# Kernel tuning notes

Hardware: AMD Instinct MI355X
Metric: run time of the kernel (lower is better)

## Reference

```python
import jax, jax.numpy as jnp
import numpy as np

N_QUBITS = 12
LAYERS = 2
BATCH = 1024


def _apply_1q(state, gate, q):
    # state: [B] + [2]*n (wire 0 = leading qubit axis); gate: [2,2] or [B,2,2]
    axis = 1 + q
    st = jnp.moveaxis(state, axis, -1)
    if gate.ndim == 2:
        st = jnp.einsum('ij,...j->...i', gate, st)
    else:  # batched gate (angle depends on the input sample)
        st = jnp.einsum('bij,b...j->b...i', gate, st)
    return jnp.moveaxis(st, -1, axis)


def _apply_cnot(state, c, t):
    # flip target axis on the control=1 slice
    ca, ta = 1 + c, 1 + t
    a0 = jnp.take(state, 0, axis=ca)
    a1 = jnp.take(state, 1, axis=ca)
    ta2 = ta - 1 if ta > ca else ta
    a1 = jnp.flip(a1, axis=ta2)
    return jnp.stack([a0, a1], axis=ca)


def _rx(a):
    # a: [B] -> gate [B,2,2]
    h = 0.5 * a
    c = jnp.cos(h).astype(jnp.complex64)
    s = (-1j) * jnp.sin(h).astype(jnp.complex64)
    return jnp.stack([jnp.stack([c, s], -1), jnp.stack([s, c], -1)], -2)


def _ry(a):
    h = 0.5 * a
    c = jnp.cos(h).astype(jnp.complex64)
    s = jnp.sin(h).astype(jnp.complex64)
    return jnp.stack([jnp.stack([c, -s], -1), jnp.stack([s, c], -1)], -2)


def _rz(a):
    h = 0.5 * a
    e0 = jnp.exp(-1j * h.astype(jnp.complex64))
    e1 = jnp.exp(1j * h.astype(jnp.complex64))
    z = jnp.zeros_like(e0)
    return jnp.stack([jnp.stack([e0, z], -1), jnp.stack([z, e1], -1)], -2)


def setup_inputs() -> dict:
    key = jax.random.key(0)
    k1, k2 = jax.random.split(key)
    x = jax.random.normal(k1, (BATCH, N_QUBITS), dtype=jnp.float32)
    theta = jax.random.normal(k2, (LAYERS, N_QUBITS, 2), dtype=jnp.float32)
    lam = jnp.ones((LAYERS, N_QUBITS), dtype=jnp.float32)
    return {"x": x, "theta": theta, "lam": lam}


def reference(x, theta, lam):
    B = x.shape[0]
    n = N_QUBITS
    # |0...0> state, batched: [B] + [2]*n
    state = jnp.zeros((B,) + (2,) * n, dtype=jnp.complex64)
    state = state.at[(slice(None),) + (0,) * n].set(1.0)
    for l in range(LAYERS):
        for q in range(n):
            state = _apply_1q(state, _rx(lam[l, q] * x[:, q]), q)
        for q in range(n):
            state = _apply_cnot(state, q, (q + 1) % n)
        for q in range(n):
            state = _apply_1q(state, _ry(theta[l, q, 0]), q)
            state = _apply_1q(state, _rz(theta[l, q, 1]), q)
    probs = state.real ** 2 + state.imag ** 2  # [B] + [2]*n
    zs = []
    for q in range(n):
        axes = tuple(i for i in range(1, n + 1) if i != 1 + q)
        p = jnp.sum(probs, axis=axes)  # [B, 2]
        zs.append(p[:, 0] - p[:, 1])   # <Z_q>
    return jnp.stack(zs, axis=1)  # [B, n_qubits]
```

## Files before the change

### kernel.cpp

```cpp
#include <hip/hip_runtime.h>
#include <math.h>

#define NQ 12
#define TPB 512


__device__ __forceinline__ int sg(int j) {
    return (j & ~15) | ((j ^ (j >> 4) ^ (j >> 8)) & 15);
}

__device__ __forceinline__ float2 pk_mul(float2 a, float2 b) {
    float2 d;
    asm("v_pk_mul_f32 %0, %1, %2" : "=v"(d) : "v"(a), "v"(b));
    return d;
}
__device__ __forceinline__ float2 pk_fma(float2 a, float2 b, float2 c) {
    float2 d;
    asm("v_pk_fma_f32 %0, %1, %2, %3" : "=v"(d) : "v"(a), "v"(b), "v"(c));
    return d;
}

#define FOR_PAIRS3(RB, STMT) do {                                     \
    const int msk_ = 1 << (RB);                                       \
    _Pragma("unroll")                                                 \
    for (int h_ = 0; h_ < 4; ++h_) {                                  \
        const int i0 = ((h_ & ~(msk_ - 1)) << 1) | (h_ & (msk_ - 1)); \
        const int i1 = i0 | msk_;                                     \
        STMT;                                                         \
    } } while (0)

#define J_A(r) (((r) << 9) | t)
#define J_B(r) (((t >> 6) << 9) | ((r) << 6) | (t & 63))
#define J_C(r) (((t >> 3) << 6) | ((r) << 3) | (t & 7))
#define J_D(r) ((t << 3) | (r))

#define LOCAL_X(JS, JD) do {                                          \
    _Pragma("unroll")                                                 \
    for (int r_ = 0; r_ < 8; ++r_) S[sg(JS(r_))] = v[r_];             \
    _Pragma("unroll")                                                 \
    for (int r_ = 0; r_ < 8; ++r_) v[r_] = S[sg(JD(r_))];             \
  } while (0)

#define M_GATE(q, RB) do {                                                  \
        float4 A4 = mA[q]; float2 P2 = mB[q];                               \
        float2 c2  = make_float2(A4.x, A4.x);                               \
        float2 s2  = make_float2(A4.y, A4.y);                               \
        float2 ms2 = make_float2(-A4.y, -A4.y);                             \
        FOR_PAIRS3(RB, {                                                    \
            float2 a1 = v[i1];                                              \
            float2 b1 = make_float2(A4.z*a1.x - A4.w*a1.y,                  \
                                    A4.z*a1.y + A4.w*a1.x);                 \
            float2 n0 = pk_fma(b1, ms2, pk_mul(v[i0], c2));                 \
            float2 n1 = pk_fma(v[i0], s2, pk_mul(b1, c2));                  \
            v[i0] = n0;                                                     \
            v[i1] = make_float2(P2.x*n1.x - P2.y*n1.y,                      \
                                P2.x*n1.y + P2.y*n1.x);                     \
        });                                                                 \
    } while (0)

#define RY_GATE(q, RB) do {                                                 \
        float2 cs = coY[q];                                                 \
        float2 c2  = make_float2(cs.x, cs.x);                               \
        float2 s2  = make_float2(cs.y, cs.y);                               \
        float2 ms2 = make_float2(-cs.y, -cs.y);                             \
        FOR_PAIRS3(RB, {                                                    \
            float2 n0 = pk_fma(v[i1], ms2, pk_mul(v[i0], c2));              \
            float2 n1 = pk_fma(v[i0], s2, pk_mul(v[i1], c2));               \
            v[i0] = n0; v[i1] = n1;                                         \
        });                                                                 \
    } while (0)

#define M_PHASE(QB)  do { _Pragma("unroll")                                 \
    for (int d_ = 0; d_ < 3; ++d_) M_GATE((QB) + d_, 2 - d_); } while (0)
#define RY_PHASE(QB) do { _Pragma("unroll")                                 \
    for (int d_ = 0; d_ < 3; ++d_) RY_GATE((QB) + d_, 2 - d_); } while (0)

__global__ __launch_bounds__(TPB) void vqc_kernel(
    const float* __restrict__ x,
    const float* __restrict__ th,
    const float* __restrict__ lm,
    float* __restrict__ out)
{
    __shared__ float2 S[4096];
    __shared__ float4 mA[12];
    __shared__ float2 mB[12];
    __shared__ float2 coI[12];
    __shared__ float2 coY[12];
    __shared__ float red[8 * 12];

    const int b = blockIdx.x;
    const int t = threadIdx.x;
    const int l = t & 63;
    const int w = t >> 6;

    if (t < 12) {
        float h = 0.5f * lm[t] * x[b * NQ + t];
        float c, s; __sincosf(h, &s, &c);
        coI[t] = make_float2(c, s);
    } else if (t < 24) {
        int q = t - 12;
        float h = 0.5f * th[24 + 2 * q];
        float c, s; __sincosf(h, &s, &c);
        coY[q] = make_float2(c, s);
    } else if (t < 36) {
        int q = t - 24;
        float ha = 0.5f * lm[12 + q] * x[b * NQ + q];
        float hy = 0.5f * th[2 * q];
        float hz = 0.5f * th[2 * q + 1];
        float ca, sa, cy, sy, cz, sz;
        __sincosf(ha, &sa, &ca);
        __sincosf(hy, &sy, &cy);
        __sincosf(hz, &sz, &cz);
        float ax = ca*cy*cz + sa*sy*sz;
        float ay = -(ca*cy*sz + sa*sy*cz);
        float bx = ca*sy*cz - sa*cy*sz;
        float by = ca*sy*sz - sa*cy*cz;
        float na = ax*ax + ay*ay, nb = bx*bx + by*by;
        float ra = rsqrtf(fmaxf(na, 1e-30f));
        float rb = rsqrtf(fmaxf(nb, 1e-30f));
        float ux = ax*ra, uy = ay*ra;
        float wx = bx*rb, wy = by*rb;
        mA[q] = make_float4(na*ra, nb*rb,
                            ux*wx - uy*wy, -(ux*wy + uy*wx));
        mB[q] = make_float2(ux*wx + uy*wy, ux*wy - uy*wx);
    }
    __syncthreads();

    float2 v[8];

    {
        const int g = (t ^ (t >> 1)) & 0x7F;
        float Pt = 1.0f;
#pragma unroll
        for (int m = 0; m < 7; ++m) {
            float2 cs = coI[8 - m];
            Pt *= ((g >> m) & 1) ? cs.y : cs.x;
        }
        const int ct = __popc(g);
        const int t0 = t & 1, t8 = (t >> 8) & 1;
        const int e1 = ((t >> 7) ^ (t >> 8)) & 1;
        float2 q11 = coI[11], q10 = coI[10], q9 = coI[9],
               q1 = coI[1], q0 = coI[0];
        const float u9  = t0 ? q9.y : q9.x;
        const float u9n = t0 ? q9.x : q9.y;
        const float u1  = e1 ? q1.y : q1.x;
        const float u1n = e1 ? q1.x : q1.y;
        const float u0  = t8 ? q0.y : q0.x;
        const float u0n = t8 ? q0.x : q0.y;
#pragma unroll
        for (int r = 0; r < 8; ++r) {
            const int r0 = r & 1, r1 = (r >> 1) & 1, r2 = (r >> 2) & 1;
            const int b11 = r0 ^ r1, b10 = r1 ^ r2;
            float m = Pt * (b11 ? q11.y : q11.x) * (b10 ? q10.y : q10.x)
                         * (r2 ? u9n : u9) * (r0 ? u1n : u1)
                         * (r0 ? u0n : u0);
            int k = (ct + b11 + b10 + (r2 ^ t0) + (r0 ^ e1) + (r0 ^ t8)) & 3;
            v[r].x = (k == 0) ? m : ((k == 2) ? -m : 0.0f);
            v[r].y = (k == 3) ? m : ((k == 1) ? -m : 0.0f);
        }
    }

    M_PHASE(9);
    LOCAL_X(J_D, J_C);
    M_PHASE(6);
    LOCAL_X(J_C, J_B);
    M_PHASE(3);
#pragma unroll
    for (int r = 0; r < 8; ++r) S[sg(J_B(r))] = v[r];
    __syncthreads();
#pragma unroll
    for (int r = 0; r < 8; ++r) v[r] = S[sg(J_A(r))];
    M_PHASE(0);

    __syncthreads();
#pragma unroll
    for (int r = 0; r < 8; ++r) {
        int j = J_A(r);
        int y = j ^ (j >> 1); y ^= y >> 2; y ^= y >> 4; y ^= y >> 8;
        int p = (y & 0x7FF) | (((__popc(j) ^ (j >> 11)) & 1) << 11);
        S[sg(p)] = v[r];
    }
    __syncthreads();
#pragma unroll
    for (int r = 0; r < 8; ++r) v[r] = S[sg(J_A(r))];

    RY_PHASE(0);
    __syncthreads();
#pragma unroll
    for (int r = 0; r < 8; ++r) S[sg(J_A(r))] = v[r];
    __syncthreads();
#pragma unroll
    for (int r = 0; r < 8; ++r) v[r] = S[sg(J_B(r))];
    RY_PHASE(3);
    LOCAL_X(J_B, J_C);
    RY_PHASE(6);
    LOCAL_X(J_C, J_D);
    RY_PHASE(9);

    float ptot = 0.f, z9 = 0.f, z10 = 0.f, z11 = 0.f;
#pragma unroll
    for (int r = 0; r < 8; ++r) {
        float p = fmaf(v[r].x, v[r].x, v[r].y * v[r].y);
        ptot += p;
        z9  += (r & 4) ? -p : p;
        z10 += (r & 2) ? -p : p;
        z11 += (r & 1) ? -p : p;
    }
    float vals[4] = {ptot, z9, z10, z11};
#pragma unroll
    for (int k = 0; k < 6; ++k) {
        const float sgn = ((l >> k) & 1) ? -1.f : 1.f;
#pragma unroll
        for (int m = 0; m < 4; ++m) {
            float tmp = __shfl_xor(vals[m], 1 << k, 64);
            vals[m] = fmaf(sgn, vals[m], tmp);
        }
    }
    if (l == 0) {
        red[w * 12 + 0]  = vals[0];
        red[w * 12 + 9]  = vals[1];
        red[w * 12 + 10] = vals[2];
        red[w * 12 + 11] = vals[3];
    } else if (__popc(l) == 1) {
        int q = 9 - __ffs(l);
        red[w * 12 + q] = vals[0];
    }
    __syncthreads();
    if (t < NQ) {
        float acc = 0.f;
#pragma unroll
        for (int ww = 0; ww < 8; ++ww) {
            float vv = red[ww * 12 + (t < 3 ? 0 : t)];
            if (t < 3) acc += ((ww >> (2 - t)) & 1) ? -vv : vv;
            else       acc += vv;
        }
        out[b * NQ + t] = acc;
    }
}

extern "C" void kernel_launch(void* const* d_in, const int* in_sizes, int n_in,
                              void* d_out, int out_size, void* d_ws, size_t ws_size,
                              hipStream_t stream) {
    const int B = in_sizes[0] / NQ;
    vqc_kernel<<<B, TPB, 0, stream>>>((const float*)d_in[0],
                                      (const float*)d_in[1],
                                      (const float*)d_in[2],
                                      (float*)d_out);
}
```

Before: 79.76 us.

## Halve block size to 256 threads with 16 amplitudes per thread

Each block now runs 256 threads, and each thread holds 16 complex amplitudes instead of 8. Each thread therefore applies four gates locally per phase, so the phases drop from four to three and one shared-memory exchange round disappears in each half. Gate coefficients are broadcast through readfirstlane so they live in scalar registers. The cost is more VGPR pressure per thread and fewer threads per block, which may lower occupancy or latency hiding.

Result: no change. 78.28 us (-1.9%).

```diff
diff --git a/kernel.cpp b/kernel.cpp
--- a/kernel.cpp
+++ b/kernel.cpp
@@ -2,11 +2,15 @@
 #include <math.h>
 
 #define NQ 12
-#define TPB 512
+#define TPB 256
 
 
 __device__ __forceinline__ int sg(int j) {
     return (j & ~15) | ((j ^ (j >> 4) ^ (j >> 8)) & 15);
+}
+
+__device__ __forceinline__ float rfl(float x) {
+    return __int_as_float(__builtin_amdgcn_readfirstlane(__float_as_int(x)));
 }
 
 __device__ __forceinline__ float2 pk_mul(float2 a, float2 b) {
@@ -20,50 +24,53 @@
     return d;
 }
 
-#define FOR_PAIRS3(RB, STMT) do {                                     \
+#define FOR_PAIRS4(RB, STMT) do {                                     \
     const int msk_ = 1 << (RB);                                       \
     _Pragma("unroll")                                                 \
-    for (int h_ = 0; h_ < 4; ++h_) {                                  \
+    for (int h_ = 0; h_ < 8; ++h_) {                                  \
         const int i0 = ((h_ & ~(msk_ - 1)) << 1) | (h_ & (msk_ - 1)); \
         const int i1 = i0 | msk_;                                     \
         STMT;                                                         \
     } } while (0)
 
-#define J_A(r) (((r) << 9) | t)
-#define J_B(r) (((t >> 6) << 9) | ((r) << 6) | (t & 63))
-#define J_C(r) (((t >> 3) << 6) | ((r) << 3) | (t & 7))
-#define J_D(r) ((t << 3) | (r))
+#define J_A(r) (((r) << 8) | t)
+#define J_B(r) (((t >> 4) << 8) | ((r) << 4) | (t & 15))
+#define J_C(r) ((t << 4) | (r))
 
 #define LOCAL_X(JS, JD) do {                                          \
     _Pragma("unroll")                                                 \
-    for (int r_ = 0; r_ < 8; ++r_) S[sg(JS(r_))] = v[r_];             \
+    for (int r_ = 0; r_ < 16; ++r_) S[sg(JS(r_))] = v[r_];            \
     _Pragma("unroll")                                                 \
-    for (int r_ = 0; r_ < 8; ++r_) v[r_] = S[sg(JD(r_))];             \
+    for (int r_ = 0; r_ < 16; ++r_) v[r_] = S[sg(JD(r_))];            \
   } while (0)
 
 #define M_GATE(q, RB) do {                                                  \
-        float4 A4 = mA[q]; float2 P2 = mB[q];                               \
-        float2 c2  = make_float2(A4.x, A4.x);                               \
-        float2 s2  = make_float2(A4.y, A4.y);                               \
-        float2 ms2 = make_float2(-A4.y, -A4.y);                             \
-        FOR_PAIRS3(RB, {                                                    \
+        float4 A4v = mA[q]; float2 P2v = mB[q];                             \
+        float az = rfl(A4v.z), aw = rfl(A4v.w);                             \
+        float px = rfl(P2v.x), py = rfl(P2v.y);                             \
+        float cth = rfl(A4v.x), sth = rfl(A4v.y);                           \
+        float2 c2  = make_float2(cth, cth);                                 \
+        float2 s2  = make_float2(sth, sth);                                 \
+        float2 ms2 = make_float2(-sth, -sth);                               \
+        FOR_PAIRS4(RB, {                                                    \
             float2 a1 = v[i1];                                              \
-            float2 b1 = make_float2(A4.z*a1.x - A4.w*a1.y,                  \
-                                    A4.z*a1.y + A4.w*a1.x);                 \
+            float2 b1 = make_float2(az*a1.x - aw*a1.y,                      \
+                                    az*a1.y + aw*a1.x);                     \
             float2 n0 = pk_fma(b1, ms2, pk_mul(v[i0], c2));                 \
             float2 n1 = pk_fma(v[i0], s2, pk_mul(b1, c2));                  \
             v[i0] = n0;                                                     \
-            v[i1] = make_float2(P2.x*n1.x - P2.y*n1.y,                      \
-                                P2.x*n1.y + P2.y*n1.x);                     \
+            v[i1] = make_float2(px*n1.x - py*n1.y,                          \
+                                px*n1.y + py*n1.x);                         \
         });                                                                 \
     } while (0)
 
 #define RY_GATE(q, RB) do {                                                 \
-        float2 cs = coY[q];                                                 \
-        float2 c2  = make_float2(cs.x, cs.x);                               \
-        float2 s2  = make_float2(cs.y, cs.y);                               \
-        float2 ms2 = make_float2(-cs.y, -cs.y);                             \
-        FOR_PAIRS3(RB, {                                                    \
+        float2 csv = coY[q];                                                \
+        float cth = rfl(csv.x), sth = rfl(csv.y);                           \
+        float2 c2  = make_float2(cth, cth);                                 \
+        float2 s2  = make_float2(sth, sth);                                 \
+        float2 ms2 = make_float2(-sth, -sth);                               \
+        FOR_PAIRS4(RB, {                                                    \
             float2 n0 = pk_fma(v[i1], ms2, pk_mul(v[i0], c2));              \
             float2 n1 = pk_fma(v[i0], s2, pk_mul(v[i1], c2));               \
             v[i0] = n0; v[i1] = n1;                                         \
@@ -71,9 +78,9 @@
     } while (0)
 
 #define M_PHASE(QB)  do { _Pragma("unroll")                                 \
-    for (int d_ = 0; d_ < 3; ++d_) M_GATE((QB) + d_, 2 - d_); } while (0)
+    for (int d_ = 0; d_ < 4; ++d_) M_GATE((QB) + d_, 3 - d_); } while (0)
 #define RY_PHASE(QB) do { _Pragma("unroll")                                 \
-    for (int d_ = 0; d_ < 3; ++d_) RY_GATE((QB) + d_, 2 - d_); } while (0)
+    for (int d_ = 0; d_ < 4; ++d_) RY_GATE((QB) + d_, 3 - d_); } while (0)
 
 __global__ __launch_bounds__(TPB) void vqc_kernel(
     const float* __restrict__ x,
@@ -86,7 +93,7 @@
     __shared__ float2 mB[12];
     __shared__ float2 coI[12];
     __shared__ float2 coY[12];
-    __shared__ float red[8 * 12];
+    __shared__ float red[4 * 12];
 
     const int b = blockIdx.x;
     const int t = threadIdx.x;
@@ -126,55 +133,54 @@
     }
     __syncthreads();
 
-    float2 v[8];
+    float2 v[16];
 
     {
-        const int g = (t ^ (t >> 1)) & 0x7F;
+        const int g = (t ^ (t >> 1)) & 0x3F;
         float Pt = 1.0f;
 #pragma unroll
-        for (int m = 0; m < 7; ++m) {
-            float2 cs = coI[8 - m];
+        for (int m = 0; m < 6; ++m) {
+            float2 cs = coI[7 - m];
             Pt *= ((g >> m) & 1) ? cs.y : cs.x;
         }
         const int ct = __popc(g);
-        const int t0 = t & 1, t8 = (t >> 8) & 1;
-        const int e1 = ((t >> 7) ^ (t >> 8)) & 1;
+        const int t0 = t & 1, t7 = (t >> 7) & 1;
+        const int e1 = ((t >> 6) ^ (t >> 7)) & 1;
         float2 q11 = coI[11], q10 = coI[10], q9 = coI[9],
-               q1 = coI[1], q0 = coI[0];
-        const float u9  = t0 ? q9.y : q9.x;
-        const float u9n = t0 ? q9.x : q9.y;
+               q8 = coI[8], q1 = coI[1], q0 = coI[0];
+        const float u8  = t0 ? q8.y : q8.x;
+        const float u8n = t0 ? q8.x : q8.y;
         const float u1  = e1 ? q1.y : q1.x;
         const float u1n = e1 ? q1.x : q1.y;
-        const float u0  = t8 ? q0.y : q0.x;
-        const float u0n = t8 ? q0.x : q0.y;
-#pragma unroll
-        for (int r = 0; r < 8; ++r) {
-            const int r0 = r & 1, r1 = (r >> 1) & 1, r2 = (r >> 2) & 1;
-            const int b11 = r0 ^ r1, b10 = r1 ^ r2;
+        const float u0  = t7 ? q0.y : q0.x;
+        const float u0n = t7 ? q0.x : q0.y;
+#pragma unroll
+        for (int r = 0; r < 16; ++r) {
+            const int r0 = r & 1, r1 = (r >> 1) & 1, r2 = (r >> 2) & 1,
+                      r3 = (r >> 3) & 1;
+            const int b11 = r0 ^ r1, b10 = r1 ^ r2, b9 = r2 ^ r3;
             float m = Pt * (b11 ? q11.y : q11.x) * (b10 ? q10.y : q10.x)
-                         * (r2 ? u9n : u9) * (r0 ? u1n : u1)
-                         * (r0 ? u0n : u0);
-            int k = (ct + b11 + b10 + (r2 ^ t0) + (r0 ^ e1) + (r0 ^ t8)) & 3;
+                         * (b9 ? q9.y : q9.x) * (r3 ? u8n : u8)
+                         * (r0 ? u1n : u1) * (r0 ? u0n : u0);
+            int k = (ct + b11 + b10 + b9 + (r3 ^ t0) + (r0 ^ e1) + (r0 ^ t7)) & 3;
             v[r].x = (k == 0) ? m : ((k == 2) ? -m : 0.0f);
             v[r].y = (k == 3) ? m : ((k == 1) ? -m : 0.0f);
         }
     }
 
-    M_PHASE(9);
-    LOCAL_X(J_D, J_C);
-    M_PHASE(6);
+    M_PHASE(8);
     LOCAL_X(J_C, J_B);
-    M_PHASE(3);
-#pragma unroll
-    for (int r = 0; r < 8; ++r) S[sg(J_B(r))] = v[r];
-    __syncthreads();
-#pragma unroll
-    for (int r = 0; r < 8; ++r) v[r] = S[sg(J_A(r))];
+    M_PHASE(4);
+#pragma unroll
+    for (int r = 0; r < 16; ++r) S[sg(J_B(r))] = v[r];
+    __syncthreads();
+#pragma unroll
+    for (int r = 0; r < 16; ++r) v[r] = S[sg(J_A(r))];
     M_PHASE(0);
 
     __syncthreads();
 #pragma unroll
-    for (int r = 0; r < 8; ++r) {
+    for (int r = 0; r < 16; ++r) {
         int j = J_A(r);
         int y = j ^ (j >> 1); y ^= y >> 2; y ^= y >> 4; y ^= y >> 8;
         int p = (y & 0x7FF) | (((__popc(j) ^ (j >> 11)) & 1) << 11);
@@ -182,57 +188,59 @@
     }
     __syncthreads();
 #pragma unroll
-    for (int r = 0; r < 8; ++r) v[r] = S[sg(J_A(r))];
+    for (int r = 0; r < 16; ++r) v[r] = S[sg(J_A(r))];
 
     RY_PHASE(0);
     __syncthreads();
 #pragma unroll
-    for (int r = 0; r < 8; ++r) S[sg(J_A(r))] = v[r];
-    __syncthreads();
-#pragma unroll
-    for (int r = 0; r < 8; ++r) v[r] = S[sg(J_B(r))];
-    RY_PHASE(3);
+    for (int r = 0; r < 16; ++r) S[sg(J_A(r))] = v[r];
+    __syncthreads();
+#pragma unroll
+    for (int r = 0; r < 16; ++r) v[r] = S[sg(J_B(r))];
+    RY_PHASE(4);
     LOCAL_X(J_B, J_C);
-    RY_PHASE(6);
-    LOCAL_X(J_C, J_D);
-    RY_PHASE(9);
-
-    float ptot = 0.f, z9 = 0.f, z10 = 0.f, z11 = 0.f;
-#pragma unroll
-    for (int r = 0; r < 8; ++r) {
+    RY_PHASE(8);
+
+    float vals[5] = {0.f, 0.f, 0.f, 0.f, 0.f};
+#pragma unroll
+    for (int r = 0; r < 16; ++r) {
         float p = fmaf(v[r].x, v[r].x, v[r].y * v[r].y);
-        ptot += p;
-        z9  += (r & 4) ? -p : p;
-        z10 += (r & 2) ? -p : p;
-        z11 += (r & 1) ? -p : p;
-    }
-    float vals[4] = {ptot, z9, z10, z11};
+        vals[0] += p;
+        vals[1] += (r & 8) ? -p : p;
+        vals[2] += (r & 4) ? -p : p;
+        vals[3] += (r & 2) ? -p : p;
+        vals[4] += (r & 1) ? -p : p;
+    }
 #pragma unroll
     for (int k = 0; k < 6; ++k) {
         const float sgn = ((l >> k) & 1) ? -1.f : 1.f;
 #pragma unroll
-        for (int m = 0; m < 4; ++m) {
+        for (int m = 0; m < 5; ++m) {
             float tmp = __shfl_xor(vals[m], 1 << k, 64);
             vals[m] = fmaf(sgn, vals[m], tmp);
         }
     }
     if (l == 0) {
         red[w * 12 + 0]  = vals[0];
-        red[w * 12 + 9]  = vals[1];
-        red[w * 12 + 10] = vals[2];
-        red[w * 12 + 11] = vals[3];
+        red[w * 12 + 8]  = vals[1];
+        red[w * 12 + 9]  = vals[2];
+        red[w * 12 + 10] = vals[3];
+        red[w * 12 + 11] = vals[4];
     } else if (__popc(l) == 1) {
-        int q = 9 - __ffs(l);
+        int q = 8 - __ffs(l);
         red[w * 12 + q] = vals[0];
     }
     __syncthreads();
     if (t < NQ) {
         float acc = 0.f;
 #pragma unroll
-        for (int ww = 0; ww < 8; ++ww) {
-            float vv = red[ww * 12 + (t < 3 ? 0 : t)];
-            if (t < 3) acc += ((ww >> (2 - t)) & 1) ? -vv : vv;
-            else       acc += vv;
+        for (int ww = 0; ww < 4; ++ww) {
+            if (t < 2) {
+                float pv = red[ww * 12 + 0];
+                acc += ((ww >> (1 - t)) & 1) ? -pv : pv;
+            } else {
+                acc += red[ww * 12 + t];
+            }
         }
         out[b * NQ + t] = acc;
     }
```
